# Kernel optimization log

Measured on AMD Instinct MI355X. Metric: run time of the kernel, lower is better.

## Reference

```python
import jax, jax.numpy as jnp
import numpy as np
from jax import lax

H = W = 496
K = 5            # gabor kernel size
WIN = 16         # window_size
STRIDE = 16
PATCH = 32
GAMMA = 0.5
PSI = np.pi / 2
THETAS = np.array([np.pi/8, np.pi/4, 3*np.pi/8, np.pi/2, 5*np.pi/8, 6*np.pi/8, 7*np.pi/8, np.pi], dtype=np.float32)


def setup_inputs() -> dict:
    key = jax.random.key(0)
    k1, k2, k3 = jax.random.split(key, 3)
    img = jax.random.normal(k1, (1, 1, H, W), dtype=jnp.float32)
    sigmas = jax.random.uniform(k2, (1, 3), dtype=jnp.float32) * 10.0   # nn.Parameter(rand*10)
    lambdas = jax.random.uniform(k3, (1, 3), dtype=jnp.float32) * np.pi  # nn.Parameter(rand*pi)
    return {"img": img, "sigmas": sigmas, "lambdas": lambdas}


def _gabor_bank(sigmas, lambdas):
    # axes: (sigma, lambda, theta, ky, kx)
    idx = jnp.arange(K, dtype=jnp.float32) - (K - 1) / 2.0
    sig = sigmas[0][:, None, None, None, None]          # [3,1,1,1,1]
    lam = lambdas[0][None, :, None, None, None]         # [1,3,1,1,1]
    th = jnp.asarray(THETAS)[None, None, :, None, None] # [1,1,8,1,1]
    y = idx[None, None, None, :, None]
    x = idx[None, None, None, None, :]
    sigma_x = sig
    sigma_y = sig / GAMMA
    sin_t, cos_t = jnp.sin(th), jnp.cos(th)
    y_theta = -x * sin_t + y * cos_t
    x_theta = x * cos_t + y * sin_t
    gb = jnp.exp(-0.5 * (x_theta**2 / sigma_x**2 + y_theta**2 / sigma_y**2)) \
         * jnp.cos(2.0 * np.pi * x_theta / lam + PSI)
    return gb.reshape(-1, 1, K, K)  # [72,1,5,5]


def reference(img, sigmas, lambdas):
    gb = _gabor_bank(sigmas, lambdas)
    res = lax.conv_general_dilated(
        img, gb, window_strides=(1, 1), padding=[(K // 2, K // 2)] * 2,
        dimension_numbers=("NCHW", "OIHW", "NCHW"))          # [1,72,H,W]
    res = res.reshape(1, 9, 8, H, W).max(axis=2)              # max over 8 thetas -> [1,9,H,W]
    out = res[0]                                              # [9,H,W]

    # find_maxima: per-channel threshold at 5*mean, zero below (torch.nn.Threshold)
    mean = out.mean(axis=(1, 2), keepdims=True)
    thr = jnp.where(out > mean * 5.0, out, 0.0)

    nw = H // STRIDE                                          # 31
    windows = thr.reshape(9, nw, WIN, nw, WIN).transpose(0, 1, 3, 2, 4).reshape(9, nw * nw, WIN * WIN)
    is_max = jnp.argmax(windows, axis=2) == (WIN * WIN) // 2  # [9, 961]

    w_idx = jnp.arange(nw * nw)
    rows = w_idx // nw * STRIDE + WIN // 2
    cols = w_idx % nw * STRIDE + WIN // 2

    # describe: zero-pad by 16, gather 32x32 patch at each candidate keypoint for every channel
    pad = jnp.pad(out, ((0, 0), (16, 16), (16, 16)))
    pr = rows[:, None, None] + jnp.arange(PATCH)[None, :, None]   # [961,32,1]
    pc = cols[:, None, None] + jnp.arange(PATCH)[None, None, :]   # [961,1,32]
    patches = pad[:, pr, pc]                                      # [9,961,32,32]

    # keep patches only for detected keypoints with nonzero content (original skips zero patches)
    valid_kp = jnp.any(is_max, axis=0)                            # [961]
    nonzero = jnp.any(patches != 0, axis=(2, 3))                  # [9,961]
    mask = (valid_kp[None, :] & nonzero).astype(patches.dtype)
    patches = patches * mask[:, :, None, None]
    return patches
```

## Files before the change

kernel.cpp:

```cpp
#include <hip/hip_runtime.h>
#include <math.h>

#define HH 496
#define WW 496
#define HWSZ (HH*WW)
#define NW 31
#define NWIN (NW*NW)

__constant__ float c_thetas[8] = {
    0.39269908169872414f, 0.7853981633974483f, 1.1780972450961724f,
    1.5707963267948966f,  1.9634954084936207f, 2.356194490192345f,
    2.748893571891069f,   3.141592653589793f};

__global__ void bank_kernel(const float* __restrict__ sigmas,
                            const float* __restrict__ lambdas,
                            float* __restrict__ filt,
                            float* __restrict__ meanacc) {
    int idx = threadIdx.x + blockIdx.x * blockDim.x;
    if (idx >= 1800) {
        if (idx < 1809) meanacc[(idx - 1800) * 16] = 0.0f;
        return;
    }
    int f = idx / 25, k = idx % 25;
    int dy = k / 5, dx = k % 5;
    int s = f / 24, rem = f % 24, l = rem / 8, t = rem % 8;
    float sig = sigmas[s], lam = lambdas[l], th = c_thetas[t];
    float y = (float)dy - 2.0f, x = (float)dx - 2.0f;
    float st = sinf(th), ct = cosf(th);
    float yt = -x * st + y * ct;
    float xt =  x * ct + y * st;
    float sx2 = sig * sig;
    float sy2 = 4.0f * sig * sig;
    float g = expf(-0.5f * (xt * xt / sx2 + yt * yt / sy2)) *
              cosf(6.28318530717958647692f * xt / lam + 1.5707963267948966f);
    filt[k * 72 + f] = g;
}

__global__ __launch_bounds__(256) void conv_kernel(
    const float* __restrict__ img, const float* __restrict__ filt,
    float* __restrict__ out, float* __restrict__ meanacc) {
    __shared__ float tile[20 * 20];
    __shared__ float red[4][9];
    int tid = threadIdx.x;
    int tx = tid & 15, ty = tid >> 4;
    int bx = blockIdx.x, by = blockIdx.y;

    for (int i = tid; i < 400; i += 256) {
        int tY = i / 20, tX = i % 20;
        int gy = by * 16 + tY - 2, gx = bx * 16 + tX - 2;
        float v = 0.0f;
        if (gy >= 0 && gy < HH && gx >= 0 && gx < WW) v = img[gy * WW + gx];
        tile[i] = v;
    }
    __syncthreads();

    float acc[72];
#pragma unroll
    for (int f = 0; f < 72; f++) acc[f] = 0.0f;

#pragma unroll
    for (int k = 0; k < 25; k++) {
        int dy = k / 5, dx = k % 5;
        float pix = tile[(ty + dy) * 20 + (tx + dx)];
        const float* fp = filt + k * 72;
#pragma unroll
        for (int f = 0; f < 72; f++) acc[f] = fmaf(pix, fp[f], acc[f]);
    }

    int y = by * 16 + ty, x = bx * 16 + tx;

    float sums[9];
#pragma unroll
    for (int c = 0; c < 9; c++) {
        float maxv = acc[c * 8];
#pragma unroll
        for (int t = 1; t < 8; t++) maxv = fmaxf(maxv, acc[c * 8 + t]);
        out[c * HWSZ + y * WW + x] = maxv;
        sums[c] = maxv;
    }

#pragma unroll
    for (int c = 0; c < 9; c++) {
        float s = sums[c];
#pragma unroll
        for (int off = 32; off > 0; off >>= 1) s += __shfl_down(s, off, 64);
        if ((tid & 63) == 0) red[tid >> 6][c] = s;
    }
    __syncthreads();
    if (tid < 9)
        atomicAdd(&meanacc[tid * 16],
                  red[0][tid] + red[1][tid] + red[2][tid] + red[3][tid]);
}

__global__ __launch_bounds__(256) void patch_kernel(
    const float* __restrict__ out, const float* __restrict__ meanacc,
    float* __restrict__ dst) {
    int w = blockIdx.x;
    int r = w / NW, cl = w % NW;
    int tid = threadIdx.x;
    int wy = tid >> 4, wx = tid & 15;
    __shared__ int lds_and[4];
    __shared__ int lds_or[4];

    int okmask = 0;
#pragma unroll
    for (int c = 0; c < 9; c++) {
        float m5 = meanacc[c * 16] * (5.0f / (float)HWSZ);
        float v  = out[c * HWSZ + (r * 16 + wy) * WW + (cl * 16 + wx)];
        float vc = out[c * HWSZ + (r * 16 + 8) * WW + (cl * 16 + 0)];
        float thr  = (v  > m5) ? v  : 0.0f;
        float thrc = (vc > m5) ? vc : 0.0f;
        bool ok = (tid < 128) ? (thr < thrc) : (thr <= thrc);
        okmask |= (ok ? 1 : 0) << c;
    }
#pragma unroll
    for (int off = 1; off < 64; off <<= 1) okmask &= __shfl_xor(okmask, off, 64);
    if ((tid & 63) == 0) lds_and[tid >> 6] = okmask;

    float vals[9][4];
    int nzmask = 0;
#pragma unroll
    for (int c = 0; c < 9; c++) {
#pragma unroll
        for (int q = 0; q < 4; q++) {
            int e = q * 256 + tid;
            int i = e >> 5, j = e & 31;
            int row = r * 16 + i - 8;
            int col = cl * 16 + j - 8;
            float v = 0.0f;
            if (row >= 0 && row < HH && col >= 0 && col < WW)
                v = out[c * HWSZ + row * WW + col];
            vals[c][q] = v;
            if (v != 0.0f) nzmask |= 1 << c;
        }
    }
#pragma unroll
    for (int off = 1; off < 64; off <<= 1) nzmask |= __shfl_xor(nzmask, off, 64);
    if ((tid & 63) == 0) lds_or[tid >> 6] = nzmask;
    __syncthreads();

    int am = lds_and[0] & lds_and[1] & lds_and[2] & lds_and[3];
    int om = lds_or[0] | lds_or[1] | lds_or[2] | lds_or[3];
    bool valid = (am != 0);

#pragma unroll
    for (int c = 0; c < 9; c++) {
        float mk = (valid && ((om >> c) & 1)) ? 1.0f : 0.0f;
#pragma unroll
        for (int q = 0; q < 4; q++) {
            int e = q * 256 + tid;
            dst[(size_t)c * NWIN * 1024 + (size_t)w * 1024 + e] = vals[c][q] * mk;
        }
    }
}

extern "C" void kernel_launch(void* const* d_in, const int* in_sizes, int n_in,
                              void* d_out, int out_size, void* d_ws, size_t ws_size,
                              hipStream_t stream) {
    const float* img     = (const float*)d_in[0];
    const float* sigmas  = (const float*)d_in[1];
    const float* lambdas = (const float*)d_in[2];
    float* ws = (float*)d_ws;
    float* filt    = ws;
    float* meanacc = ws + 2048;
    float* outb    = ws + 4096;

    bank_kernel<<<8, 256, 0, stream>>>(sigmas, lambdas, filt, meanacc);
    conv_kernel<<<dim3(NW, NW), 256, 0, stream>>>(img, filt, outb, meanacc);
    patch_kernel<<<NWIN, 256, 0, stream>>>(outb, meanacc, (float*)d_out);
}
```

Measured before the change: 130.1 us.

## Split conv across channel groups and separate validity check from vectorized patch copy

The conv grid gains a z dimension of 3, so each block computes 24 filters (3 output channels) instead of 72. This cuts register pressure and triples the number of blocks. The old patch kernel is split in two: a small kernel computes the per-window keypoint validity, and a copy kernel with a 961x9 grid handles one channel per block using float4 loads and stores plus __syncthreads_or for the nonzero test. In exchange there is an extra kernel launch, and each conv block reloads the image tile three times.

```diff
diff --git a/kernel.cpp b/kernel.cpp
--- a/kernel.cpp
+++ b/kernel.cpp
@@ -40,10 +40,10 @@
     const float* __restrict__ img, const float* __restrict__ filt,
     float* __restrict__ out, float* __restrict__ meanacc) {
     __shared__ float tile[20 * 20];
-    __shared__ float red[4][9];
+    __shared__ float red[4][3];
     int tid = threadIdx.x;
     int tx = tid & 15, ty = tid >> 4;
-    int bx = blockIdx.x, by = blockIdx.y;
+    int bx = blockIdx.x, by = blockIdx.y, cg = blockIdx.z;
 
     for (int i = tid; i < 400; i += 256) {
         int tY = i / 20, tX = i % 20;
@@ -54,53 +54,52 @@
     }
     __syncthreads();
 
-    float acc[72];
+    float acc[24];
 #pragma unroll
-    for (int f = 0; f < 72; f++) acc[f] = 0.0f;
+    for (int f = 0; f < 24; f++) acc[f] = 0.0f;
 
 #pragma unroll
     for (int k = 0; k < 25; k++) {
         int dy = k / 5, dx = k % 5;
         float pix = tile[(ty + dy) * 20 + (tx + dx)];
-        const float* fp = filt + k * 72;
+        const float* fp = filt + k * 72 + cg * 24;
 #pragma unroll
-        for (int f = 0; f < 72; f++) acc[f] = fmaf(pix, fp[f], acc[f]);
+        for (int f = 0; f < 24; f++) acc[f] = fmaf(pix, fp[f], acc[f]);
     }
 
     int y = by * 16 + ty, x = bx * 16 + tx;
 
-    float sums[9];
+    float sums[3];
 #pragma unroll
-    for (int c = 0; c < 9; c++) {
-        float maxv = acc[c * 8];
+    for (int cc = 0; cc < 3; cc++) {
+        float maxv = acc[cc * 8];
 #pragma unroll
-        for (int t = 1; t < 8; t++) maxv = fmaxf(maxv, acc[c * 8 + t]);
-        out[c * HWSZ + y * WW + x] = maxv;
-        sums[c] = maxv;
+        for (int t = 1; t < 8; t++) maxv = fmaxf(maxv, acc[cc * 8 + t]);
+        out[(cg * 3 + cc) * HWSZ + y * WW + x] = maxv;
+        sums[cc] = maxv;
     }
 
 #pragma unroll
-    for (int c = 0; c < 9; c++) {
-        float s = sums[c];
+    for (int cc = 0; cc < 3; cc++) {
+        float s = sums[cc];
 #pragma unroll
         for (int off = 32; off > 0; off >>= 1) s += __shfl_down(s, off, 64);
-        if ((tid & 63) == 0) red[tid >> 6][c] = s;
+        if ((tid & 63) == 0) red[tid >> 6][cc] = s;
     }
     __syncthreads();
-    if (tid < 9)
-        atomicAdd(&meanacc[tid * 16],
+    if (tid < 3)
+        atomicAdd(&meanacc[(cg * 3 + tid) * 16],
                   red[0][tid] + red[1][tid] + red[2][tid] + red[3][tid]);
 }
 
-__global__ __launch_bounds__(256) void patch_kernel(
+__global__ __launch_bounds__(256) void valid_kernel(
     const float* __restrict__ out, const float* __restrict__ meanacc,
-    float* __restrict__ dst) {
+    int* __restrict__ valid) {
     int w = blockIdx.x;
     int r = w / NW, cl = w % NW;
     int tid = threadIdx.x;
     int wy = tid >> 4, wx = tid & 15;
     __shared__ int lds_and[4];
-    __shared__ int lds_or[4];
 
     int okmask = 0;
 #pragma unroll
@@ -116,42 +115,32 @@
 #pragma unroll
     for (int off = 1; off < 64; off <<= 1) okmask &= __shfl_xor(okmask, off, 64);
     if ((tid & 63) == 0) lds_and[tid >> 6] = okmask;
+    __syncthreads();
+    if (tid == 0)
+        valid[w] = (lds_and[0] & lds_and[1] & lds_and[2] & lds_and[3]) != 0 ? 1 : 0;
+}
 
-    float vals[9][4];
-    int nzmask = 0;
-#pragma unroll
-    for (int c = 0; c < 9; c++) {
-#pragma unroll
-        for (int q = 0; q < 4; q++) {
-            int e = q * 256 + tid;
-            int i = e >> 5, j = e & 31;
-            int row = r * 16 + i - 8;
-            int col = cl * 16 + j - 8;
-            float v = 0.0f;
-            if (row >= 0 && row < HH && col >= 0 && col < WW)
-                v = out[c * HWSZ + row * WW + col];
-            vals[c][q] = v;
-            if (v != 0.0f) nzmask |= 1 << c;
-        }
+__global__ __launch_bounds__(256) void patch_copy_kernel(
+    const float* __restrict__ out, const int* __restrict__ valid,
+    float* __restrict__ dst) {
+    int w = blockIdx.x, c = blockIdx.y;
+    int r = w / NW, cl = w % NW;
+    int tid = threadIdx.x;
+    int i = tid >> 3;
+    int jg = (tid & 7) << 2;
+
+    int row = r * 16 + i - 8;
+    int col = cl * 16 + jg - 8;
+    float4 v = make_float4(0.f, 0.f, 0.f, 0.f);
+    if (row >= 0 && row < HH && col >= 0) {
+        if (col + 3 < WW)
+            v = *(const float4*)(out + (size_t)c * HWSZ + (size_t)row * WW + col);
     }
-#pragma unroll
-    for (int off = 1; off < 64; off <<= 1) nzmask |= __shfl_xor(nzmask, off, 64);
-    if ((tid & 63) == 0) lds_or[tid >> 6] = nzmask;
-    __syncthreads();
-
-    int am = lds_and[0] & lds_and[1] & lds_and[2] & lds_and[3];
-    int om = lds_or[0] | lds_or[1] | lds_or[2] | lds_or[3];
-    bool valid = (am != 0);
-
-#pragma unroll
-    for (int c = 0; c < 9; c++) {
-        float mk = (valid && ((om >> c) & 1)) ? 1.0f : 0.0f;
-#pragma unroll
-        for (int q = 0; q < 4; q++) {
-            int e = q * 256 + tid;
-            dst[(size_t)c * NWIN * 1024 + (size_t)w * 1024 + e] = vals[c][q] * mk;
-        }
-    }
+    bool nzl = (v.x != 0.f) || (v.y != 0.f) || (v.z != 0.f) || (v.w != 0.f);
+    int nz = __syncthreads_or(nzl ? 1 : 0);
+    float mk = (valid[w] && nz) ? 1.0f : 0.0f;
+    v.x *= mk; v.y *= mk; v.z *= mk; v.w *= mk;
+    *(float4*)(dst + (size_t)c * NWIN * 1024 + (size_t)w * 1024 + i * 32 + jg) = v;
 }
 
 extern "C" void kernel_launch(void* const* d_in, const int* in_sizes, int n_in,
@@ -163,9 +152,11 @@
     float* ws = (float*)d_ws;
     float* filt    = ws;
     float* meanacc = ws + 2048;
+    int*   valid   = (int*)(ws + 2240);
     float* outb    = ws + 4096;
 
     bank_kernel<<<8, 256, 0, stream>>>(sigmas, lambdas, filt, meanacc);
-    conv_kernel<<<dim3(NW, NW), 256, 0, stream>>>(img, filt, outb, meanacc);
-    patch_kernel<<<NWIN, 256, 0, stream>>>(outb, meanacc, (float*)d_out);
+    conv_kernel<<<dim3(NW, NW, 3), 256, 0, stream>>>(img, filt, outb, meanacc);
+    valid_kernel<<<NWIN, 256, 0, stream>>>(outb, meanacc, valid);
+    patch_copy_kernel<<<dim3(NWIN, 9), 256, 0, stream>>>(outb, valid, (float*)d_out);
 }
```

Result: faster. 125.6 us (-3.4%).
